# Kernel optimization log

Measured on AMD Instinct MI355X. Metric: run time of the kernel, lower is better.

Reference implementation:

```python
import jax, jax.numpy as jnp
import numpy as np


def _head_configs(n_heads, patch_num):
    candidates = set()
    for d in range(1, patch_num + 1):
        for K in (3, 5, 7):
            eff = (K - 1) * d + 1
            if eff <= patch_num and K <= patch_num and (K % 2 == 1):
                candidates.add((K, d, eff))
    gk = patch_num if patch_num % 2 == 1 else patch_num - 1
    gk = max(1, gk)
    candidates.add((gk, 1, gk))
    cand = sorted(candidates, key=lambda x: (x[2], -x[0], x[1]))
    if not cand:
        return [(1, 1)] * n_heads
    configs = []
    for h in range(n_heads):
        idx = round(h * (len(cand) - 1) / max(1, n_heads - 1))
        idx = min(idx, len(cand) - 1)
        configs.append((cand[idx][0], cand[idx][1]))
    return configs


def _build_na_mask(n_heads, patch_num):
    # [H, N, N] bool: True where key position is a (dilated) neighbor of query
    mask = np.zeros((n_heads, patch_num, patch_num), dtype=bool)
    pos = np.arange(patch_num)
    for h, (K, d) in enumerate(_head_configs(n_heads, patch_num)):
        off = (np.arange(K) - K // 2) * d
        ideal = pos[:, None] + off[None, :]          # [N, K]
        nb = np.clip(ideal, 0, patch_num - 1)
        valid = (ideal >= 0) & (ideal < patch_num)
        rows = np.repeat(pos, K)
        mask[h, rows[valid.ravel()], nb.ravel()[valid.ravel()]] = True
    return mask


N_HEADS = 16
PATCH_NUM = 1024
HEAD_DIM = 64
BATCH = 8


def setup_inputs() -> dict:
    key = jax.random.key(0)
    kq, kk, kv = jax.random.split(key, 3)
    shape = (BATCH, PATCH_NUM, N_HEADS, HEAD_DIM)  # [B, L, H, E]
    queries = jax.random.normal(kq, shape, dtype=jnp.float32)
    keys = jax.random.normal(kk, shape, dtype=jnp.float32)
    values = jax.random.normal(kv, shape, dtype=jnp.float32)
    na_mask = jnp.asarray(_build_na_mask(N_HEADS, PATCH_NUM))  # [H, N, N] bool
    return {"queries": queries, "keys": keys, "values": values, "na_mask": na_mask}


def reference(queries, keys, values, na_mask):
    B, L, H, E = queries.shape
    scale = E ** (-0.5)
    q = jnp.transpose(queries, (0, 2, 1, 3))  # [B, H, N, E]
    k = jnp.transpose(keys, (0, 2, 1, 3))
    v = jnp.transpose(values, (0, 2, 1, 3))
    attn = jnp.einsum('bhne,bhme->bhnm', q, k) * scale  # [B, H, N, N]
    attn = jnp.where(na_mask[None], attn, -jnp.inf)
    attn = jax.nn.softmax(attn, axis=-1)
    out = jnp.einsum('bhnm,bhme->bhne', attn, v)
    return jnp.transpose(out, (0, 2, 1, 3))  # [B, L, H, E]
```

## Files before the change

kernel.cpp:

```cpp
#include <hip/hip_runtime.h>

#define B_ 8
#define L_ 1024
#define H_ 16
#define E_ 64

__constant__ int HK[16] = {3, 3, 3, 3, 7, 3, 3, 7, 3, 5, 7, 3, 5, 7, 5, 3};
__constant__ int HD[16] = {1, 35, 69, 103, 46, 171, 205, 80, 273, 154, 114, 375, 205, 148, 239, 511};

__global__ __launch_bounds__(256)
void msna_fwd(const float* __restrict__ Q, const float* __restrict__ Kp,
              const float* __restrict__ Vp, float* __restrict__ O)
{
    const int nwg = B_ * H_ * (L_ / 16);
    const int cpx = nwg >> 3;
    int blk = blockIdx.x;
    blk = (blk & 7) * cpx + (blk >> 3);

    const int tid  = threadIdx.x;
    const int lane = tid & 15;
    const int qi   = tid >> 4;
    const int qt   = blk & 63;
    const int h    = (blk >> 6) & 15;
    const int b    = blk >> 10;
    const int q    = qt * 16 + qi;

    const int Kh   = HK[h];
    const int Dh   = HD[h];
    const int half = Kh >> 1;

    const size_t rowbase = (size_t)b * (L_ * H_ * E_) + h * E_ + 4 * lane;

    int   mm[7];
    bool  val[7];
#pragma unroll
    for (int jj = 0; jj < 7; ++jj) {
        const int j = jj - 3;
        const int m = q + j * Dh;
        val[jj] = (j >= -half) && (j <= half) && (m >= 0) && (m < L_);
        mm[jj]  = m < 0 ? 0 : (m >= L_ ? L_ - 1 : m);
    }

    const float4 qv = *reinterpret_cast<const float4*>(Q + rowbase + (size_t)q * (H_ * E_));
    float4 kv[7], vv[7];
#pragma unroll
    for (int jj = 0; jj < 7; ++jj)
        kv[jj] = *reinterpret_cast<const float4*>(Kp + rowbase + (size_t)mm[jj] * (H_ * E_));
#pragma unroll
    for (int jj = 0; jj < 7; ++jj)
        vv[jj] = *reinterpret_cast<const float4*>(Vp + rowbase + (size_t)mm[jj] * (H_ * E_));

    float sc[7];
#pragma unroll
    for (int jj = 0; jj < 7; ++jj) {
        float d = qv.x * kv[jj].x + qv.y * kv[jj].y + qv.z * kv[jj].z + qv.w * kv[jj].w;
        d += __shfl_xor(d, 1);
        d += __shfl_xor(d, 2);
        d += __shfl_xor(d, 4);
        d += __shfl_xor(d, 8);
        sc[jj] = val[jj] ? d * 0.125f : -1e30f;
    }

    float mx = sc[0];
#pragma unroll
    for (int jj = 1; jj < 7; ++jj) mx = fmaxf(mx, sc[jj]);

    float e[7];
    float sum = 0.f;
#pragma unroll
    for (int jj = 0; jj < 7; ++jj) {
        e[jj] = __expf(sc[jj] - mx);
        sum += e[jj];
    }
    const float inv = 1.f / sum;

    float4 acc = make_float4(0.f, 0.f, 0.f, 0.f);
#pragma unroll
    for (int jj = 0; jj < 7; ++jj) {
        const float w = e[jj] * inv;
        acc.x += w * vv[jj].x;
        acc.y += w * vv[jj].y;
        acc.z += w * vv[jj].z;
        acc.w += w * vv[jj].w;
    }

    *reinterpret_cast<float4*>(O + rowbase + (size_t)q * (H_ * E_)) = acc;
}

extern "C" void kernel_launch(void* const* d_in, const int* in_sizes, int n_in,
                              void* d_out, int out_size, void* d_ws, size_t ws_size,
                              hipStream_t stream)
{
    const float* Q = (const float*)d_in[0];
    const float* K = (const float*)d_in[1];
    const float* V = (const float*)d_in[2];
    float* O = (float*)d_out;

    const int blocks = B_ * H_ * (L_ / 16);
    msna_fwd<<<blocks, 256, 0, stream>>>(Q, K, V, O);
}
```

Baseline: 28.30 us.

## Specialize per-head kernel size via templates and use DPP row reductions

The kernel now dispatches to a template instantiated for the head's neighborhood half-width (1, 2 or 3), so heads with 3 or 5 neighbors no longer load and compute all 7 K/V rows. Before, the clamped out-of-window rows were loaded anyway and then masked. The cross-lane shuffle reductions become DPP row_shr adds, index math moves from size_t to 32-bit ints, and launch bounds add an occupancy hint. The cost is more code through three instantiations and a per-block branch, though that branch is uniform across the block.

```diff
diff --git a/kernel.cpp b/kernel.cpp
--- a/kernel.cpp
+++ b/kernel.cpp
@@ -4,11 +4,88 @@
 #define L_ 1024
 #define H_ 16
 #define E_ 64
+#define HE_ (H_ * E_)
 
-__constant__ int HK[16] = {3, 3, 3, 3, 7, 3, 3, 7, 3, 5, 7, 3, 5, 7, 5, 3};
-__constant__ int HD[16] = {1, 35, 69, 103, 46, 171, 205, 80, 273, 154, 114, 375, 205, 148, 239, 511};
+__constant__ int HHALF[16] = {1, 1, 1, 1, 3, 1, 1, 3, 1, 2, 3, 1, 2, 3, 2, 1};
+__constant__ int HD[16]    = {1, 35, 69, 103, 46, 171, 205, 80, 273, 154, 114, 375, 205, 148, 239, 511};
 
-__global__ __launch_bounds__(256)
+template <int CTRL>
+__device__ __forceinline__ float dpp_add(float x) {
+    int moved = __builtin_amdgcn_update_dpp(0, __float_as_int(x), CTRL, 0xf, 0xf, false);
+    return x + __int_as_float(moved);
+}
+__device__ __forceinline__ float row16_sum(float x) {
+    x = dpp_add<0x121>(x);
+    x = dpp_add<0x122>(x);
+    x = dpp_add<0x124>(x);
+    x = dpp_add<0x128>(x);
+    return x;
+}
+
+template <int HALF>
+__device__ __forceinline__ void run_head(const float* __restrict__ Q,
+                                         const float* __restrict__ Kp,
+                                         const float* __restrict__ Vp,
+                                         float* __restrict__ O,
+                                         int rowbase, int q, int Dh)
+{
+    constexpr int NS = 2 * HALF + 1;
+    const int qoff = rowbase + q * HE_;
+
+    int  moff[NS];
+    bool val[NS];
+#pragma unroll
+    for (int jj = 0; jj < NS; ++jj) {
+        const int j = jj - HALF;
+        const int m = q + j * Dh;
+        val[jj] = (m >= 0) && (m < L_);
+        const int mc = m < 0 ? 0 : (m >= L_ ? L_ - 1 : m);
+        moff[jj] = rowbase + mc * HE_;
+    }
+
+    const float4 qv = *reinterpret_cast<const float4*>(Q + qoff);
+    float4 kv[NS], vv[NS];
+#pragma unroll
+    for (int jj = 0; jj < NS; ++jj)
+        kv[jj] = *reinterpret_cast<const float4*>(Kp + moff[jj]);
+#pragma unroll
+    for (int jj = 0; jj < NS; ++jj)
+        vv[jj] = *reinterpret_cast<const float4*>(Vp + moff[jj]);
+
+    float sc[NS];
+#pragma unroll
+    for (int jj = 0; jj < NS; ++jj) {
+        float d = qv.x * kv[jj].x + qv.y * kv[jj].y + qv.z * kv[jj].z + qv.w * kv[jj].w;
+        d = row16_sum(d);
+        sc[jj] = val[jj] ? d * 0.125f : -1e30f;
+    }
+
+    float mx = sc[0];
+#pragma unroll
+    for (int jj = 1; jj < NS; ++jj) mx = fmaxf(mx, sc[jj]);
+    float e[NS];
+    float sum = 0.f;
+#pragma unroll
+    for (int jj = 0; jj < NS; ++jj) {
+        e[jj] = __expf(sc[jj] - mx);
+        sum += e[jj];
+    }
+    const float inv = 1.f / sum;
+
+    float4 acc = make_float4(0.f, 0.f, 0.f, 0.f);
+#pragma unroll
+    for (int jj = 0; jj < NS; ++jj) {
+        const float w = e[jj] * inv;
+        acc.x += w * vv[jj].x;
+        acc.y += w * vv[jj].y;
+        acc.z += w * vv[jj].z;
+        acc.w += w * vv[jj].w;
+    }
+
+    *reinterpret_cast<float4*>(O + qoff) = acc;
+}
+
+__global__ __launch_bounds__(256, 4)
 void msna_fwd(const float* __restrict__ Q, const float* __restrict__ Kp,
               const float* __restrict__ Vp, float* __restrict__ O)
 {
@@ -25,66 +102,13 @@
     const int b    = blk >> 10;
     const int q    = qt * 16 + qi;
 
-    const int Kh   = HK[h];
-    const int Dh   = HD[h];
-    const int half = Kh >> 1;
+    const int Dh = HD[h];
+    const int hf = HHALF[h];
+    const int rowbase = b * (L_ * HE_) + h * E_ + 4 * lane;
 
-    const size_t rowbase = (size_t)b * (L_ * H_ * E_) + h * E_ + 4 * lane;
-
-    int   mm[7];
-    bool  val[7];
-#pragma unroll
-    for (int jj = 0; jj < 7; ++jj) {
-        const int j = jj - 3;
-        const int m = q + j * Dh;
-        val[jj] = (j >= -half) && (j <= half) && (m >= 0) && (m < L_);
-        mm[jj]  = m < 0 ? 0 : (m >= L_ ? L_ - 1 : m);
-    }
-
-    const float4 qv = *reinterpret_cast<const float4*>(Q + rowbase + (size_t)q * (H_ * E_));
-    float4 kv[7], vv[7];
-#pragma unroll
-    for (int jj = 0; jj < 7; ++jj)
-        kv[jj] = *reinterpret_cast<const float4*>(Kp + rowbase + (size_t)mm[jj] * (H_ * E_));
-#pragma unroll
-    for (int jj = 0; jj < 7; ++jj)
-        vv[jj] = *reinterpret_cast<const float4*>(Vp + rowbase + (size_t)mm[jj] * (H_ * E_));
-
-    float sc[7];
-#pragma unroll
-    for (int jj = 0; jj < 7; ++jj) {
-        float d = qv.x * kv[jj].x + qv.y * kv[jj].y + qv.z * kv[jj].z + qv.w * kv[jj].w;
-        d += __shfl_xor(d, 1);
-        d += __shfl_xor(d, 2);
-        d += __shfl_xor(d, 4);
-        d += __shfl_xor(d, 8);
-        sc[jj] = val[jj] ? d * 0.125f : -1e30f;
-    }
-
-    float mx = sc[0];
-#pragma unroll
-    for (int jj = 1; jj < 7; ++jj) mx = fmaxf(mx, sc[jj]);
-
-    float e[7];
-    float sum = 0.f;
-#pragma unroll
-    for (int jj = 0; jj < 7; ++jj) {
-        e[jj] = __expf(sc[jj] - mx);
-        sum += e[jj];
-    }
-    const float inv = 1.f / sum;
-
-    float4 acc = make_float4(0.f, 0.f, 0.f, 0.f);
-#pragma unroll
-    for (int jj = 0; jj < 7; ++jj) {
-        const float w = e[jj] * inv;
-        acc.x += w * vv[jj].x;
-        acc.y += w * vv[jj].y;
-        acc.z += w * vv[jj].z;
-        acc.w += w * vv[jj].w;
-    }
-
-    *reinterpret_cast<float4*>(O + rowbase + (size_t)q * (H_ * E_)) = acc;
+    if (hf == 1)      run_head<1>(Q, Kp, Vp, O, rowbase, q, Dh);
+    else if (hf == 2) run_head<2>(Q, Kp, Vp, O, rowbase, q, Dh);
+    else              run_head<3>(Q, Kp, Vp, O, rowbase, q, Dh);
 }
 
 extern "C" void kernel_launch(void* const* d_in, const int* in_sizes, int n_in,
```

Result: faster. 25.59 us (-9.6%).

## Loop over eight heads per block and use DPP row reductions

Applied to the files above, without the earlier changes.

Each block now handles a 16-row tile for eight heads in an unrolled loop, which cuts the grid from 8192 to 1024 blocks. The XCD swizzle is adjusted to match. The cross-lane dot-product reduction uses DPP row_shr adds in place of shfl_xor, avoiding LDS-based shuffles. In exchange there is less parallelism per launch and longer serial work per thread. Rows loaded by neighbouring heads are adjacent in memory, so coalescing may improve, and the int offsets replace size_t.

```diff
diff --git a/kernel.cpp b/kernel.cpp
--- a/kernel.cpp
+++ b/kernel.cpp
@@ -4,87 +4,92 @@
 #define L_ 1024
 #define H_ 16
 #define E_ 64
+#define HE_ (H_ * E_)
 
-__constant__ int HK[16] = {3, 3, 3, 3, 7, 3, 3, 7, 3, 5, 7, 3, 5, 7, 5, 3};
-__constant__ int HD[16] = {1, 35, 69, 103, 46, 171, 205, 80, 273, 154, 114, 375, 205, 148, 239, 511};
+__constant__ int HHALF[16] = {1,1,1,1,3,1,1,3,1,2,3,1,2,3,2,1};
+__constant__ int HD[16]    = {1,35,69,103,46,171,205,80,273,154,114,375,205,148,239,511};
+
+template <int CTRL>
+__device__ __forceinline__ float dpp_add(float x) {
+    int moved = __builtin_amdgcn_update_dpp(0, __float_as_int(x), CTRL, 0xf, 0xf, false);
+    return x + __int_as_float(moved);
+}
+__device__ __forceinline__ float row16_sum(float x) {
+    x = dpp_add<0x121>(x);
+    x = dpp_add<0x122>(x);
+    x = dpp_add<0x124>(x);
+    x = dpp_add<0x128>(x);
+    return x;
+}
 
 __global__ __launch_bounds__(256)
 void msna_fwd(const float* __restrict__ Q, const float* __restrict__ Kp,
               const float* __restrict__ Vp, float* __restrict__ O)
 {
-    const int nwg = B_ * H_ * (L_ / 16);
-    const int cpx = nwg >> 3;
-    int blk = blockIdx.x;
-    blk = (blk & 7) * cpx + (blk >> 3);
+    const int x = blockIdx.x;
+    const int blk = (x & 7) * 128 + (x >> 3);
 
-    const int tid  = threadIdx.x;
-    const int lane = tid & 15;
-    const int qi   = tid >> 4;
-    const int qt   = blk & 63;
-    const int h    = (blk >> 6) & 15;
-    const int b    = blk >> 10;
-    const int q    = qt * 16 + qi;
+    const int hb   = (blk & 1) * 8;
+    const int tile = (blk >> 1) & 63;
+    const int b    = blk >> 7;
 
-    const int Kh   = HK[h];
-    const int Dh   = HD[h];
-    const int half = Kh >> 1;
+    const int lane = threadIdx.x & 15;
+    const int slot = threadIdx.x >> 4;
+    const int l    = tile * 16 + slot;
 
-    const size_t rowbase = (size_t)b * (L_ * H_ * E_) + h * E_ + 4 * lane;
+#pragma unroll 2
+    for (int i = 0; i < 8; ++i) {
+        const int h    = hb + i;
+        const int d    = HD[h];
+        const int half = HHALF[h];
+        const int base = b * (L_ * HE_) + h * E_ + 4 * lane;
+        const int qoff = base + l * HE_;
 
-    int   mm[7];
-    bool  val[7];
+        const float4 qv = *reinterpret_cast<const float4*>(Q + qoff);
+
+        float4 kv[7], vv[7];
+        bool ok[7];
 #pragma unroll
-    for (int jj = 0; jj < 7; ++jj) {
-        const int j = jj - 3;
-        const int m = q + j * Dh;
-        val[jj] = (j >= -half) && (j <= half) && (m >= 0) && (m < L_);
-        mm[jj]  = m < 0 ? 0 : (m >= L_ ? L_ - 1 : m);
+        for (int jj = 0; jj < 7; ++jj) {
+            const int j = jj - 3;
+            const int m = l + j * d;
+            ok[jj] = (j >= -half) && (j <= half) && (m >= 0) && (m < L_);
+            const int mc = m < 0 ? 0 : (m >= L_ - 1 ? L_ - 1 : m);
+            kv[jj] = *reinterpret_cast<const float4*>(Kp + base + mc * HE_);
+            vv[jj] = *reinterpret_cast<const float4*>(Vp + base + mc * HE_);
+        }
+
+        float sc[7];
+#pragma unroll
+        for (int jj = 0; jj < 7; ++jj) {
+            float dd = qv.x * kv[jj].x + qv.y * kv[jj].y +
+                       qv.z * kv[jj].z + qv.w * kv[jj].w;
+            dd = row16_sum(dd);
+            sc[jj] = ok[jj] ? dd * 0.125f : -1e30f;
+        }
+
+        float mx = sc[0];
+#pragma unroll
+        for (int jj = 1; jj < 7; ++jj) mx = fmaxf(mx, sc[jj]);
+        float e[7];
+        float sum = 0.f;
+#pragma unroll
+        for (int jj = 0; jj < 7; ++jj) {
+            e[jj] = __expf(sc[jj] - mx);
+            sum += e[jj];
+        }
+        const float inv = 1.f / sum;
+
+        float4 acc = make_float4(0.f, 0.f, 0.f, 0.f);
+#pragma unroll
+        for (int jj = 0; jj < 7; ++jj) {
+            const float w = e[jj] * inv;
+            acc.x += w * vv[jj].x; acc.y += w * vv[jj].y;
+            acc.z += w * vv[jj].z; acc.w += w * vv[jj].w;
+        }
+
+        *reinterpret_cast<float4*>(O + qoff) = acc;
     }
-
-    const float4 qv = *reinterpret_cast<const float4*>(Q + rowbase + (size_t)q * (H_ * E_));
-    float4 kv[7], vv[7];
-#pragma unroll
-    for (int jj = 0; jj < 7; ++jj)
-        kv[jj] = *reinterpret_cast<const float4*>(Kp + rowbase + (size_t)mm[jj] * (H_ * E_));
-#pragma unroll
-    for (int jj = 0; jj < 7; ++jj)
-        vv[jj] = *reinterpret_cast<const float4*>(Vp + rowbase + (size_t)mm[jj] * (H_ * E_));
-
-    float sc[7];
-#pragma unroll
-    for (int jj = 0; jj < 7; ++jj) {
-        float d = qv.x * kv[jj].x + qv.y * kv[jj].y + qv.z * kv[jj].z + qv.w * kv[jj].w;
-        d += __shfl_xor(d, 1);
-        d += __shfl_xor(d, 2);
-        d += __shfl_xor(d, 4);
-        d += __shfl_xor(d, 8);
-        sc[jj] = val[jj] ? d * 0.125f : -1e30f;
-    }
-
-    float mx = sc[0];
-#pragma unroll
-    for (int jj = 1; jj < 7; ++jj) mx = fmaxf(mx, sc[jj]);
-
-    float e[7];
-    float sum = 0.f;
-#pragma unroll
-    for (int jj = 0; jj < 7; ++jj) {
-        e[jj] = __expf(sc[jj] - mx);
-        sum += e[jj];
-    }
-    const float inv = 1.f / sum;
-
-    float4 acc = make_float4(0.f, 0.f, 0.f, 0.f);
-#pragma unroll
-    for (int jj = 0; jj < 7; ++jj) {
-        const float w = e[jj] * inv;
-        acc.x += w * vv[jj].x;
-        acc.y += w * vv[jj].y;
-        acc.z += w * vv[jj].z;
-        acc.w += w * vv[jj].w;
-    }
-
-    *reinterpret_cast<float4*>(O + rowbase + (size_t)q * (H_ * E_)) = acc;
 }
 
 extern "C" void kernel_launch(void* const* d_in, const int* in_sizes, int n_in,
@@ -96,6 +101,6 @@
     const float* V = (const float*)d_in[2];
     float* O = (float*)d_out;
 
-    const int blocks = B_ * H_ * (L_ / 16);
+    const int blocks = B_ * 64 * 2;
     msna_fwd<<<blocks, 256, 0, stream>>>(Q, K, V, O);
 }
```

New measurement: 30.23 us. +6.8%, slower.
